# Optimization experiments

Measured on AMD Instinct MI355X. Metric: run time of the kernel, lower is better.

## Reference

```python
import jax, jax.numpy as jnp
import numpy as np

N_NODES = 100000
N_EDGES = 600000
H = 128          # hidden_units
LH = 256         # lin_hidden_units
F_IN = 3         # num_features (x, y, area)
C = 8            # out_classes


def setup_inputs() -> dict:
    key = jax.random.key(0)
    ks = jax.random.split(key, 12)
    s = 0.05
    return {
        "x": jax.random.normal(ks[0], (N_NODES, F_IN), dtype=jnp.float32),
        "edge_index": jax.random.randint(ks[1], (2, N_EDGES), 0, N_NODES, dtype=jnp.int64),
        # conv1: lin_l (aggregated neighbors, has bias), lin_r (root, no bias)
        "Wl1": jax.random.normal(ks[2], (H, F_IN), dtype=jnp.float32) * s,
        "bl1": jnp.zeros((H,), dtype=jnp.float32),
        "Wr1": jax.random.normal(ks[3], (H, F_IN), dtype=jnp.float32) * s,
        # conv2
        "Wl2": jax.random.normal(ks[4], (H, H), dtype=jnp.float32) * s,
        "bl2": jnp.zeros((H,), dtype=jnp.float32),
        "Wr2": jax.random.normal(ks[5], (H, H), dtype=jnp.float32) * s,
        # MLP head
        "W1": jax.random.normal(ks[6], (LH, H), dtype=jnp.float32) * s,
        "b1": jnp.zeros((LH,), dtype=jnp.float32),
        "W2": jax.random.normal(ks[7], (C, LH), dtype=jnp.float32) * s,
        "b2": jnp.zeros((C,), dtype=jnp.float32),
    }


def _normalize(x):
    coords = x[:, :2]                      # [N, 2]
    areas = x[:, 2:3]                      # [N, 1]
    mx = jnp.max(coords, axis=0)
    mn = jnp.min(coords, axis=0)
    theta = jnp.float32(np.pi / 2)
    c, sn = jnp.cos(theta), jnp.sin(theta)
    R = jnp.array([[1.0, 0.0], [0.0, 1.0]], dtype=x.dtype) * c + \
        jnp.array([[0.0, -1.0], [1.0, 0.0]], dtype=x.dtype) * sn
    rotated = coords @ R.T                 # (R @ coords.T).T
    rotate = (mx[1] - mn[1]) > (mx[0] - mn[0])
    coords = jnp.where(rotate, rotated, coords)
    coords = (coords - jnp.mean(coords, axis=0)) / jnp.max(coords, axis=0)
    areas = areas / jnp.max(areas, axis=0)
    return jnp.concatenate([coords, areas], axis=-1)


def _sage_conv(x, src, dst, Wl, bl, Wr):
    # mean aggregation of source features at target nodes
    msg = x[src]                                               # [E, d] gather
    agg = jax.ops.segment_sum(msg, dst, num_segments=N_NODES)  # [N, d]
    deg = jax.ops.segment_sum(jnp.ones((src.shape[0],), x.dtype), dst,
                              num_segments=N_NODES)
    agg = agg / jnp.maximum(deg, 1.0)[:, None]
    return agg @ Wl.T + bl + x @ Wr.T


def reference(x, edge_index, Wl1, bl1, Wr1, Wl2, bl2, Wr2, W1, b1, W2, b2):
    src, dst = edge_index[0], edge_index[1]
    h = _normalize(x)
    h = jnp.tanh(_sage_conv(h, src, dst, Wl1, bl1, Wr1))
    h = jnp.tanh(_sage_conv(h, src, dst, Wl2, bl2, Wr2))
    h = jnp.tanh(h @ W1.T + b1)
    h = h @ W2.T + b2
    return jax.nn.softmax(h, axis=1)
```

## Files before the change

### kernel.cpp

```cpp
#include <hip/hip_runtime.h>
#include <hip/hip_bf16.h>
#include <math.h>

#define N_NODES 100000
#define N_EDGES 600000
#define H 128
#define LH 256
#define CDIM 8
#define NB_STATS 256
#define NT128 ((N_NODES + 127) / 128)
#define ELLW 64
#define NB_NODE ((N_NODES + 255) / 256)

#define NBUCK 391
#define NBLK_P1 64
#define EPB (N_EDGES / NBLK_P1)
#define CAP 72

typedef __attribute__((ext_vector_type(8))) short short8;
typedef __attribute__((ext_vector_type(4))) float floatx4;

#define OFF_PART   0
#define OFF_DEG    2816
#define OFF_H0     (OFF_DEG + N_NODES)
#define OFF_ELL    (OFF_H0 + N_NODES*4)
#define OFF_CNTT   (OFF_ELL + N_NODES*ELLW)
#define OFF_SCR    (OFF_CNTT + NBUCK*NBLK_P1)
#define OFF_WPK2   (OFF_SCR + NBUCK*NBLK_P1*CAP*2)
#define OFF_WPK1   (OFF_WPK2 + 16384)
#define OFF_W2PK   (OFF_WPK1 + 16384)
#define OFF_XB     (OFF_W2PK + 2048)

__device__ __forceinline__ float rot_c() { return cosf(1.57079632679489661923f); }
__device__ __forceinline__ float rot_s() { return sinf(1.57079632679489661923f); }
__device__ __forceinline__ float bfhi(unsigned v) { return __uint_as_float(v & 0xffff0000u); }
__device__ __forceinline__ float bflo(unsigned v) { return __uint_as_float(v << 16); }
__device__ __forceinline__ unsigned short bfu(float f) {
    __hip_bfloat16 h = __float2bfloat16(f);
    return *(unsigned short*)&h;
}
__device__ __forceinline__ float ftanh(float x) {
    float e = __expf(2.0f * x);
    return 1.0f - 2.0f * __builtin_amdgcn_rcpf(e + 1.0f);
}

__global__ __launch_bounds__(256) void statsPart_k(const float* __restrict__ x,
        float* __restrict__ part, const int* __restrict__ ei,
        int* __restrict__ cntT, int2* __restrict__ scratch) {
    __shared__ float red[4][11];
    __shared__ int lcnt[NBUCK];
    int tid = threadIdx.x;

    if (blockIdx.x >= NB_STATS) {
        int blk = blockIdx.x - NB_STATS;
        for (int i = tid; i < NBUCK; i += 256) lcnt[i] = 0;
        __syncthreads();
        int base = blk * EPB;
        for (int e = base + tid; e < base + EPB; e += 256) {
            int s = ei[e], d = ei[N_EDGES + e];
            int b = d >> 8;
            int pos = atomicAdd(&lcnt[b], 1);
            scratch[(b * NBLK_P1 + blk) * CAP + pos] = make_int2(s, d);
        }
        __syncthreads();
        for (int i = tid; i < NBUCK; i += 256)
            cntT[i * NBLK_P1 + blk] = lcnt[i];
        return;
    }

    const float c = rot_c(), sn = rot_s();
    float mn0 = INFINITY, mx0 = -INFINITY, mn1 = INFINITY, mx1 = -INFINITY;
    float s0 = 0.f, s1 = 0.f, sr0 = 0.f, sr1 = 0.f;
    float mxr0 = -INFINITY, mxr1 = -INFINITY, mxa = -INFINITY;
    for (int i = blockIdx.x * 256 + tid; i < N_NODES; i += NB_STATS * 256) {
        float x0 = x[3*i], x1 = x[3*i+1], a = x[3*i+2];
        float r0 = c*x0 - sn*x1;
        float r1 = sn*x0 + c*x1;
        mn0 = fminf(mn0, x0); mx0 = fmaxf(mx0, x0);
        mn1 = fminf(mn1, x1); mx1 = fmaxf(mx1, x1);
        s0 += x0; s1 += x1; sr0 += r0; sr1 += r1;
        mxr0 = fmaxf(mxr0, r0); mxr1 = fmaxf(mxr1, r1);
        mxa = fmaxf(mxa, a);
    }
    float vals[11] = {mn0, mx0, mn1, mx1, s0, s1, sr0, sr1, mxr0, mxr1, mxa};
    int lane = tid & 63, wave = tid >> 6;
    #pragma unroll
    for (int v = 0; v < 11; v++) {
        const int op = (v==0||v==2) ? 0 : (v>=4 && v<=7) ? 2 : 1;
        float val = vals[v];
        #pragma unroll
        for (int off = 32; off > 0; off >>= 1) {
            float o = __shfl_down(val, off);
            val = (op==0) ? fminf(val,o) : (op==1) ? fmaxf(val,o) : (val+o);
        }
        if (lane == 0) red[wave][v] = val;
    }
    __syncthreads();
    if (tid < 11) {
        int v = tid;
        int op = (v==0||v==2) ? 0 : (v>=4 && v<=7) ? 2 : 1;
        float a = red[0][v], b = red[1][v], cc = red[2][v], d = red[3][v];
        float r = (op==0) ? fminf(fminf(a,b), fminf(cc,d))
                : (op==1) ? fmaxf(fmaxf(a,b), fmaxf(cc,d))
                : (a + b + cc + d);
        part[blockIdx.x * 11 + v] = r;
    }
}

__global__ __launch_bounds__(256) void binNorm_k(const float* __restrict__ x,
        const float* __restrict__ part, float4* __restrict__ h0,
        const float* __restrict__ Wl2, const float* __restrict__ Wr2,
        const float* __restrict__ W1, const float* __restrict__ W2,
        __hip_bfloat16* __restrict__ Wpk2, __hip_bfloat16* __restrict__ Wpk1,
        __hip_bfloat16* __restrict__ W2pk,
        const int* __restrict__ cntT, const int2* __restrict__ scratch,
        int* __restrict__ ell, int* __restrict__ deg) {
    __shared__ int pref[NBLK_P1 + 1];
    __shared__ int ncnt[256];
    __shared__ float res[11];
    int tid = threadIdx.x;

    if (blockIdx.x < NBUCK) {
        int b = blockIdx.x;
        ncnt[tid] = 0;
        if (tid < NBLK_P1) pref[tid + 1] = cntT[b * NBLK_P1 + tid];
        __syncthreads();
        if (tid == 0) {
            pref[0] = 0;
            int acc = 0;
            #pragma unroll 8
            for (int j = 0; j < NBLK_P1; j++) { acc += pref[j+1]; pref[j+1] = acc; }
        }
        __syncthreads();
        int T = pref[NBLK_P1];
        for (int f = tid; f < T; f += 256) {
            int lo = 0, hi = NBLK_P1;
            while (hi - lo > 1) {
                int mid = (lo + hi) >> 1;
                if (pref[mid] <= f) lo = mid; else hi = mid;
            }
            int2 sd = scratch[(b * NBLK_P1 + lo) * CAP + (f - pref[lo])];
            int pos = atomicAdd(&ncnt[sd.y & 255], 1);
            ell[(sd.y << 6) + pos] = sd.x;
        }
        __syncthreads();
        int n = (b << 8) + tid;
        if (n < N_NODES) deg[n] = ncnt[tid];
        return;
    }

    int nb = blockIdx.x - NBUCK;
    int i = nb * 256 + tid;
    if (tid < 64) {
        const int ops[11] = {0,1,0,1,2,2,2,2,1,1,1};
        for (int v = 0; v < 11; v++) {
            float val = part[tid * 11 + v];
            #pragma unroll
            for (int p = 1; p < 4; p++) {
                float o = part[(tid + p*64) * 11 + v];
                val = (ops[v]==0) ? fminf(val,o) : (ops[v]==1) ? fmaxf(val,o) : (val+o);
            }
            #pragma unroll
            for (int off = 32; off > 0; off >>= 1) {
                float o = __shfl_down(val, off);
                val = (ops[v]==0) ? fminf(val,o) : (ops[v]==1) ? fmaxf(val,o) : (val+o);
            }
            if (tid == 0) res[v] = val;
        }
    }
    __syncthreads();
    int rotate = (res[3] - res[2]) > (res[1] - res[0]);
    float mean0 = (rotate ? res[6] : res[4]) / (float)N_NODES;
    float mean1 = (rotate ? res[7] : res[5]) / (float)N_NODES;
    float imx0  = 1.0f / (rotate ? res[8] : res[1]);
    float imx1  = 1.0f / (rotate ? res[9] : res[3]);
    float imxa  = 1.0f / res[10];

    if (i < N_NODES) {
        const float c = rot_c(), sn = rot_s();
        float x0 = x[3*i], x1 = x[3*i+1], a = x[3*i+2];
        float u0 = rotate ? (c*x0 - sn*x1) : x0;
        float u1 = rotate ? (sn*x0 + c*x1) : x1;
        h0[i] = make_float4((u0 - mean0) * imx0, (u1 - mean1) * imx1, a * imxa, 0.f);
    }
    int idx = i;
    if (idx < 32768) {
        int j = idx & 7, lane = (idx >> 3) & 63, nt = (idx >> 9) & 7, ks = idx >> 12;
        int k = ks*32 + (lane >> 4)*8 + j;
        int n = nt*16 + (lane & 15);
        float v = (k < 128) ? Wl2[n*H + k] : Wr2[n*H + (k - 128)];
        Wpk2[idx] = __float2bfloat16(v);
    } else if (idx < 65536) {
        int i2 = idx - 32768;
        int j = i2 & 7, lane = (i2 >> 3) & 63, nt = (i2 >> 9) & 15, ks = i2 >> 13;
        int k = ks*32 + (lane >> 4)*8 + j;
        int n = nt*16 + (lane & 15);
        Wpk1[i2] = __float2bfloat16(W1[n*H + k]);
    } else if (idx < 69632) {
        int i3 = idx - 65536;
        int j = i3 & 7, lane = (i3 >> 3) & 63, ks = i3 >> 9;
        int k = ks*32 + (lane >> 4)*8 + j;
        int n = lane & 15;
        W2pk[i3] = __float2bfloat16((n < CDIM) ? W2[n*LH + k] : 0.f);
    }
}

__global__ __launch_bounds__(256) void agg1conv1_k(const float4* __restrict__ h0,
        const int* __restrict__ deg, const int* __restrict__ ell,
        const float* __restrict__ Wl1, const float* __restrict__ bl1,
        const float* __restrict__ Wr1, __hip_bfloat16* __restrict__ Xb) {
    __shared__ float wl[H*3], wr[H*3], bb[H];
    __shared__ float4 sa[256];
    int tid = threadIdx.x;
    for (int i = tid; i < H*3; i += 256) { wl[i] = Wl1[i]; wr[i] = Wr1[i]; }
    if (tid < H) bb[tid] = bl1[tid];
    int base = blockIdx.x * 256;
    int n = base + tid;
    float4 av = make_float4(0.f, 0.f, 0.f, 0.f);
    if (n < N_NODES) {
        int dg = deg[n];
        int start = n << 6, end = start + dg;
        float a0 = 0.f, a1 = 0.f, a2 = 0.f;
        int e = start;
        for (; e + 3 < end; e += 4) {
            int s0 = ell[e], s1 = ell[e+1], s2 = ell[e+2], s3 = ell[e+3];
            float4 v0 = h0[s0];
            float4 v1 = h0[s1];
            float4 v2 = h0[s2];
            float4 v3 = h0[s3];
            a0 += (v0.x + v1.x) + (v2.x + v3.x);
            a1 += (v0.y + v1.y) + (v2.y + v3.y);
            a2 += (v0.z + v1.z) + (v2.z + v3.z);
        }
        for (; e < end; e++) {
            float4 v = h0[ell[e]];
            a0 += v.x; a1 += v.y; a2 += v.z;
        }
        float inv = 1.0f / (float)max(dg, 1);
        av = make_float4(a0 * inv, a1 * inv, a2 * inv, 0.f);
    }
    sa[tid] = av;
    __syncthreads();
    int sub = tid >> 6;
    int j2 = (tid & 63) * 2;
    for (int i = 0; i < 64; i++) {
        int loc = i * 4 + sub;
        int nn = base + loc;
        if (nn >= N_NODES) break;
        float4 a = sa[loc];
        float4 xv = h0[nn];
        float o0 = wl[3*j2+0]*a.x + wl[3*j2+1]*a.y + wl[3*j2+2]*a.z + bb[j2]
                 + wr[3*j2+0]*xv.x + wr[3*j2+1]*xv.y + wr[3*j2+2]*xv.z;
        float o1 = wl[3*j2+3]*a.x + wl[3*j2+4]*a.y + wl[3*j2+5]*a.z + bb[j2+1]
                 + wr[3*j2+3]*xv.x + wr[3*j2+4]*xv.y + wr[3*j2+5]*xv.z;
        unsigned pv = ((unsigned)bfu(ftanh(o1)) << 16) | (unsigned)bfu(ftanh(o0));
        *(unsigned*)&Xb[(size_t)nn*256 + 128 + j2] = pv;
    }
}

__global__ void agg2_k(__hip_bfloat16* __restrict__ Xb, const int* __restrict__ deg,
                       const int* __restrict__ ell) {
    int lane = threadIdx.x & 15;
    int n = blockIdx.x * 16 + (threadIdx.x >> 4);
    int dg = deg[n];
    int start = n << 6, end = start + dg;
    const short* XbS = (const short*)Xb;
    float a0=0.f,a1=0.f,a2=0.f,a3=0.f,a4=0.f,a5=0.f,a6=0.f,a7=0.f;
    int e = start;
    for (; e + 1 < end; e += 2) {
        int s0 = ell[e], s1 = ell[e+1];
        uint4 v0 = *(const uint4*)&XbS[(size_t)s0*256 + 128 + lane*8];
        uint4 v1 = *(const uint4*)&XbS[(size_t)s1*256 + 128 + lane*8];
        a0 += bflo(v0.x) + bflo(v1.x); a1 += bfhi(v0.x) + bfhi(v1.x);
        a2 += bflo(v0.y) + bflo(v1.y); a3 += bfhi(v0.y) + bfhi(v1.y);
        a4 += bflo(v0.z) + bflo(v1.z); a5 += bfhi(v0.z) + bfhi(v1.z);
        a6 += bflo(v0.w) + bflo(v1.w); a7 += bfhi(v0.w) + bfhi(v1.w);
    }
    if (e < end) {
        int s0 = ell[e];
        uint4 v0 = *(const uint4*)&XbS[(size_t)s0*256 + 128 + lane*8];
        a0 += bflo(v0.x); a1 += bfhi(v0.x);
        a2 += bflo(v0.y); a3 += bfhi(v0.y);
        a4 += bflo(v0.z); a5 += bfhi(v0.z);
        a6 += bflo(v0.w); a7 += bfhi(v0.w);
    }
    float inv = 1.0f / (float)max(dg, 1);
    uint4 o;
    o.x = ((unsigned)bfu(a1*inv) << 16) | (unsigned)bfu(a0*inv);
    o.y = ((unsigned)bfu(a3*inv) << 16) | (unsigned)bfu(a2*inv);
    o.z = ((unsigned)bfu(a5*inv) << 16) | (unsigned)bfu(a4*inv);
    o.w = ((unsigned)bfu(a7*inv) << 16) | (unsigned)bfu(a6*inv);
    *(uint4*)&Xb[(size_t)n*256 + lane*8] = o;
}

__global__ __launch_bounds__(512, 4) void conv2mlp_k(const __hip_bfloat16* __restrict__ Xb,
        const __hip_bfloat16* __restrict__ Wpk2, const float* __restrict__ bl2,
        const __hip_bfloat16* __restrict__ Wpk1, const float* __restrict__ b1,
        const __hip_bfloat16* __restrict__ W2pk, const float* __restrict__ b2,
        float* __restrict__ out) {
    __shared__ short Cs[8 * 16 * 128];
    int tid = threadIdx.x;
    int lane = tid & 63, wave = tid >> 6;
    int quad = lane >> 4, m = lane & 15, c0 = lane & 15;
    short* Tw = &Cs[wave * (16 * 128)];
    const short* Bg2 = (const short*)Wpk2;
    const short* Bg1 = (const short*)Wpk1;
    const short* Bg0 = (const short*)W2pk;

    int tile = blockIdx.x;
    short8 areg[8];
    {
        int row = tile*128 + wave*16 + m;
        int rowL = row < N_NODES ? row : N_NODES - 1;
        const short* Arow = (const short*)Xb + (size_t)rowL * 256;
        #pragma unroll
        for (int ks = 0; ks < 8; ks++)
            areg[ks] = *(const short8*)(Arow + ks*32 + quad*8);
    }
    floatx4 acc2[8];
    #pragma unroll
    for (int i = 0; i < 8; i++)
        #pragma unroll
        for (int r = 0; r < 4; r++) acc2[i][r] = 0.f;
    #pragma unroll
    for (int ks = 0; ks < 8; ks++) {
        #pragma unroll
        for (int nt = 0; nt < 8; nt++) {
            short8 b = *(const short8*)&Bg2[((ks*8 + nt)*64 + lane)*8];
            acc2[nt] = __builtin_amdgcn_mfma_f32_16x16x32_bf16(areg[ks], b, acc2[nt], 0, 0, 0);
        }
    }
    #pragma unroll
    for (int nt = 0; nt < 8; nt++) {
        float bl2v = bl2[nt*16 + c0];
        int cg = nt*2 + (c0 >> 3);
        #pragma unroll
        for (int r = 0; r < 4; r++) {
            int row = quad*4 + r;
            Tw[row*128 + ((cg ^ row) << 3) + (c0 & 7)] =
                (short)bfu(ftanh(acc2[nt][r] + bl2v));
        }
    }
    floatx4 acc1[16];
    #pragma unroll
    for (int i = 0; i < 16; i++)
        #pragma unroll
        for (int r = 0; r < 4; r++) acc1[i][r] = 0.f;
    #pragma unroll
    for (int ks = 0; ks < 4; ks++) {
        short8 a = *(const short8*)&Tw[m*128 + (((ks*4 + quad) ^ m) << 3)];
        #pragma unroll
        for (int nt = 0; nt < 16; nt++) {
            short8 b = *(const short8*)&Bg1[((ks*16 + nt)*64 + lane)*8];
            acc1[nt] = __builtin_amdgcn_mfma_f32_16x16x32_bf16(a, b, acc1[nt], 0, 0, 0);
        }
    }
    floatx4 lacc;
    #pragma unroll
    for (int r = 0; r < 4; r++) lacc[r] = 0.f;
    #pragma unroll
    for (int ch = 0; ch < 4; ch++) {
        #pragma unroll
        for (int ntl = 0; ntl < 4; ntl++) {
            int nt = ch*4 + ntl;
            float b1v = b1[nt*16 + c0];
            int cg = ntl*2 + (c0 >> 3);
            #pragma unroll
            for (int r = 0; r < 4; r++) {
                int row = quad*4 + r;
                Tw[row*128 + ((cg ^ row) << 3) + (c0 & 7)] =
                    (short)bfu(ftanh(acc1[nt][r] + b1v));
            }
        }
        #pragma unroll
        for (int k2 = 0; k2 < 2; k2++) {
            short8 a = *(const short8*)&Tw[m*128 + (((k2*4 + quad) ^ m) << 3)];
            short8 w2 = *(const short8*)&Bg0[((ch*2 + k2)*64 + lane)*8];
            lacc = __builtin_amdgcn_mfma_f32_16x16x32_bf16(a, w2, lacc, 0, 0, 0);
        }
    }
    float b2v = (c0 < CDIM) ? b2[c0] : 0.f;
    int rbase = tile*128 + wave*16 + quad*4;
    #pragma unroll
    for (int r = 0; r < 4; r++) {
        float v = lacc[r] + b2v;
        float mval = (c0 < CDIM) ? v : -INFINITY;
        #pragma unroll
        for (int off = 1; off < 8; off <<= 1)
            mval = fmaxf(mval, __shfl_xor(mval, off));
        float e = (c0 < CDIM) ? __expf(v - mval) : 0.f;
        float ssum = e;
        #pragma unroll
        for (int off = 1; off < 8; off <<= 1)
            ssum += __shfl_xor(ssum, off);
        int rowg = rbase + r;
        if (c0 < CDIM && rowg < N_NODES)
            out[(size_t)rowg*CDIM + c0] = e / ssum;
    }
}

extern "C" void kernel_launch(void* const* d_in, const int* in_sizes, int n_in,
                              void* d_out, int out_size, void* d_ws, size_t ws_size,
                              hipStream_t stream) {
    const float* x   = (const float*)d_in[0];
    const int*   ei  = (const int*)d_in[1];
    const float* Wl1 = (const float*)d_in[2];
    const float* bl1 = (const float*)d_in[3];
    const float* Wr1 = (const float*)d_in[4];
    const float* Wl2 = (const float*)d_in[5];
    const float* bl2 = (const float*)d_in[6];
    const float* Wr2 = (const float*)d_in[7];
    const float* W1  = (const float*)d_in[8];
    const float* b1  = (const float*)d_in[9];
    const float* W2  = (const float*)d_in[10];
    const float* b2  = (const float*)d_in[11];

    float* ws     = (float*)d_ws;
    float* part   = ws + OFF_PART;
    int*   deg    = (int*)(ws + OFF_DEG);
    float4* h0    = (float4*)(ws + OFF_H0);
    int*   ell    = (int*)(ws + OFF_ELL);
    int*   cntT   = (int*)(ws + OFF_CNTT);
    int2*  scratch= (int2*)(ws + OFF_SCR);
    __hip_bfloat16* Wpk2 = (__hip_bfloat16*)(ws + OFF_WPK2);
    __hip_bfloat16* Wpk1 = (__hip_bfloat16*)(ws + OFF_WPK1);
    __hip_bfloat16* W2pk = (__hip_bfloat16*)(ws + OFF_W2PK);
    __hip_bfloat16* Xb   = (__hip_bfloat16*)(ws + OFF_XB);

    statsPart_k<<<NB_STATS + NBLK_P1, 256, 0, stream>>>(x, part, ei, cntT, scratch);
    binNorm_k<<<NBUCK + NB_NODE, 256, 0, stream>>>(x, part, h0,
            Wl2, Wr2, W1, W2, Wpk2, Wpk1, W2pk, cntT, scratch, ell, deg);
    agg1conv1_k<<<NB_NODE, 256, 0, stream>>>(h0, deg, ell,
            Wl1, bl1, Wr1, Xb);
    agg2_k<<<N_NODES / 16, 256, 0, stream>>>(Xb, deg, ell);
    conv2mlp_k<<<NT128, 512, 0, stream>>>(Xb, Wpk2, bl2, Wpk1, b1, W2pk, b2,
            (float*)d_out);
}
```

Before: 219.5 us.

## Stage W1 weights in LDS and shrink per-wave activation staging to padded slices

Each block now copies the packed 64KB W1 weight matrix into shared memory once, so MLP layer-1 B operands come from LDS rather than global memory. The conv2 and layer-1 tanh outputs are written to LDS in 32-column chunks, each just before the MFMA k-step that reads it, using a 40-short padded row stride instead of a full 128-wide swizzled tile. This cuts per-wave staging memory and interleaves the activation math with the matmuls. The cost is about 74KB of shared memory per block, which likely lowers occupancy below the launch-bounds target, plus an extra block-wide sync for the weight copy.

```diff
diff --git a/kernel.cpp b/kernel.cpp
--- a/kernel.cpp
+++ b/kernel.cpp
@@ -293,18 +293,26 @@
     *(uint4*)&Xb[(size_t)n*256 + lane*8] = o;
 }
 
+#define SLICE 640
 __global__ __launch_bounds__(512, 4) void conv2mlp_k(const __hip_bfloat16* __restrict__ Xb,
         const __hip_bfloat16* __restrict__ Wpk2, const float* __restrict__ bl2,
         const __hip_bfloat16* __restrict__ Wpk1, const float* __restrict__ b1,
         const __hip_bfloat16* __restrict__ W2pk, const float* __restrict__ b2,
         float* __restrict__ out) {
-    __shared__ short Cs[8 * 16 * 128];
+    __shared__ short Ws1[32768];
+    __shared__ short Cs[8 * SLICE];
     int tid = threadIdx.x;
     int lane = tid & 63, wave = tid >> 6;
     int quad = lane >> 4, m = lane & 15, c0 = lane & 15;
-    short* Tw = &Cs[wave * (16 * 128)];
+    {
+        const float4* s1 = (const float4*)Wpk1;
+        float4* d1 = (float4*)Ws1;
+        #pragma unroll
+        for (int i = 0; i < 8; i++) d1[tid + i*512] = s1[tid + i*512];
+    }
+    __syncthreads();
+    short* Tw = &Cs[wave * SLICE];
     const short* Bg2 = (const short*)Wpk2;
-    const short* Bg1 = (const short*)Wpk1;
     const short* Bg0 = (const short*)W2pk;
 
     int tile = blockIdx.x;
@@ -330,17 +338,6 @@
             acc2[nt] = __builtin_amdgcn_mfma_f32_16x16x32_bf16(areg[ks], b, acc2[nt], 0, 0, 0);
         }
     }
-    #pragma unroll
-    for (int nt = 0; nt < 8; nt++) {
-        float bl2v = bl2[nt*16 + c0];
-        int cg = nt*2 + (c0 >> 3);
-        #pragma unroll
-        for (int r = 0; r < 4; r++) {
-            int row = quad*4 + r;
-            Tw[row*128 + ((cg ^ row) << 3) + (c0 & 7)] =
-                (short)bfu(ftanh(acc2[nt][r] + bl2v));
-        }
-    }
     floatx4 acc1[16];
     #pragma unroll
     for (int i = 0; i < 16; i++)
@@ -348,10 +345,19 @@
         for (int r = 0; r < 4; r++) acc1[i][r] = 0.f;
     #pragma unroll
     for (int ks = 0; ks < 4; ks++) {
-        short8 a = *(const short8*)&Tw[m*128 + (((ks*4 + quad) ^ m) << 3)];
+        #pragma unroll
+        for (int p = 0; p < 2; p++) {
+            int nt = ks*2 + p;
+            float bl2v = bl2[nt*16 + c0];
+            int lc = p*16 + c0;
+            #pragma unroll
+            for (int r = 0; r < 4; r++)
+                Tw[(quad*4 + r)*40 + lc] = (short)bfu(ftanh(acc2[nt][r] + bl2v));
+        }
+        short8 a = *(const short8*)&Tw[m*40 + quad*8];
         #pragma unroll
         for (int nt = 0; nt < 16; nt++) {
-            short8 b = *(const short8*)&Bg1[((ks*16 + nt)*64 + lane)*8];
+            short8 b = *(const short8*)&Ws1[((ks*16 + nt)*64 + lane)*8];
             acc1[nt] = __builtin_amdgcn_mfma_f32_16x16x32_bf16(a, b, acc1[nt], 0, 0, 0);
         }
     }
@@ -359,25 +365,19 @@
     #pragma unroll
     for (int r = 0; r < 4; r++) lacc[r] = 0.f;
     #pragma unroll
-    for (int ch = 0; ch < 4; ch++) {
-        #pragma unroll
-        for (int ntl = 0; ntl < 4; ntl++) {
-            int nt = ch*4 + ntl;
+    for (int ch = 0; ch < 8; ch++) {
+        #pragma unroll
+        for (int p = 0; p < 2; p++) {
+            int nt = ch*2 + p;
             float b1v = b1[nt*16 + c0];
-            int cg = ntl*2 + (c0 >> 3);
+            int lc = p*16 + c0;
             #pragma unroll
-            for (int r = 0; r < 4; r++) {
-                int row = quad*4 + r;
-                Tw[row*128 + ((cg ^ row) << 3) + (c0 & 7)] =
-                    (short)bfu(ftanh(acc1[nt][r] + b1v));
-            }
-        }
-        #pragma unroll
-        for (int k2 = 0; k2 < 2; k2++) {
-            short8 a = *(const short8*)&Tw[m*128 + (((k2*4 + quad) ^ m) << 3)];
-            short8 w2 = *(const short8*)&Bg0[((ch*2 + k2)*64 + lane)*8];
-            lacc = __builtin_amdgcn_mfma_f32_16x16x32_bf16(a, w2, lacc, 0, 0, 0);
-        }
+            for (int r = 0; r < 4; r++)
+                Tw[(quad*4 + r)*40 + lc] = (short)bfu(ftanh(acc1[nt][r] + b1v));
+        }
+        short8 a = *(const short8*)&Tw[m*40 + quad*8];
+        short8 w2 = *(const short8*)&Bg0[(ch*64 + lane)*8];
+        lacc = __builtin_amdgcn_mfma_f32_16x16x32_bf16(a, w2, lacc, 0, 0, 0);
     }
     float b2v = (c0 < CDIM) ? b2[c0] : 0.f;
     int rbase = tile*128 + wave*16 + quad*4;
```

After: 209.4 us. 1.05x faster.

## Process two 16-row groups per wave in conv2+MLP kernel to reuse weight fragments

Applied to the files above, without the earlier changes.

The fused conv2+MLP kernel now launches 256 threads per block, and each wave handles 32 rows as two 16-row groups. Every weight B-fragment loaded from global memory feeds two MFMAs, which halves weight load traffic per row. The 256-wide hidden layer is split into two passes of 128 columns, and each 32-column slice is staged through a small per-wave LDS buffer so the W2 projection runs incrementally. The cost is more accumulator registers per wave and lower occupancy (launch bounds 256,2), which can limit latency hiding.

```diff
diff --git a/kernel.cpp b/kernel.cpp
--- a/kernel.cpp
+++ b/kernel.cpp
@@ -293,41 +293,45 @@
     *(uint4*)&Xb[(size_t)n*256 + lane*8] = o;
 }
 
-__global__ __launch_bounds__(512, 4) void conv2mlp_k(const __hip_bfloat16* __restrict__ Xb,
+__global__ __launch_bounds__(256, 2) void conv2mlp_k(const __hip_bfloat16* __restrict__ Xb,
         const __hip_bfloat16* __restrict__ Wpk2, const float* __restrict__ bl2,
         const __hip_bfloat16* __restrict__ Wpk1, const float* __restrict__ b1,
         const __hip_bfloat16* __restrict__ W2pk, const float* __restrict__ b2,
         float* __restrict__ out) {
-    __shared__ short Cs[8 * 16 * 128];
+    __shared__ short Hs[4 * 2 * 2048];
+    __shared__ short Ms[4 * 640];
     int tid = threadIdx.x;
     int lane = tid & 63, wave = tid >> 6;
     int quad = lane >> 4, m = lane & 15, c0 = lane & 15;
-    short* Tw = &Cs[wave * (16 * 128)];
+    short* Hw = &Hs[wave * 4096];
+    short* Tw = &Ms[wave * 640];
     const short* Bg2 = (const short*)Wpk2;
     const short* Bg1 = (const short*)Wpk1;
     const short* Bg0 = (const short*)W2pk;
 
     int tile = blockIdx.x;
-    short8 areg[8];
-    {
-        int row = tile*128 + wave*16 + m;
-        int rowL = row < N_NODES ? row : N_NODES - 1;
-        const short* Arow = (const short*)Xb + (size_t)rowL * 256;
-        #pragma unroll
-        for (int ks = 0; ks < 8; ks++)
-            areg[ks] = *(const short8*)(Arow + ks*32 + quad*8);
-    }
-    floatx4 acc2[8];
+    int rbase0 = tile*128 + wave*32;
+    int r0 = rbase0 + m;            r0 = r0 < N_NODES ? r0 : N_NODES - 1;
+    int r1 = rbase0 + 16 + m;       r1 = r1 < N_NODES ? r1 : N_NODES - 1;
+    const short* Arow0 = (const short*)Xb + (size_t)r0 * 256;
+    const short* Arow1 = (const short*)Xb + (size_t)r1 * 256;
+
+    floatx4 acc2[8][2];
     #pragma unroll
     for (int i = 0; i < 8; i++)
         #pragma unroll
-        for (int r = 0; r < 4; r++) acc2[i][r] = 0.f;
+        for (int rg = 0; rg < 2; rg++)
+            #pragma unroll
+            for (int r = 0; r < 4; r++) acc2[i][rg][r] = 0.f;
     #pragma unroll
     for (int ks = 0; ks < 8; ks++) {
+        short8 a0 = *(const short8*)(Arow0 + ks*32 + quad*8);
+        short8 a1 = *(const short8*)(Arow1 + ks*32 + quad*8);
         #pragma unroll
         for (int nt = 0; nt < 8; nt++) {
             short8 b = *(const short8*)&Bg2[((ks*8 + nt)*64 + lane)*8];
-            acc2[nt] = __builtin_amdgcn_mfma_f32_16x16x32_bf16(areg[ks], b, acc2[nt], 0, 0, 0);
+            acc2[nt][0] = __builtin_amdgcn_mfma_f32_16x16x32_bf16(a0, b, acc2[nt][0], 0, 0, 0);
+            acc2[nt][1] = __builtin_amdgcn_mfma_f32_16x16x32_bf16(a1, b, acc2[nt][1], 0, 0, 0);
         }
     }
     #pragma unroll
@@ -335,67 +339,82 @@
         float bl2v = bl2[nt*16 + c0];
         int cg = nt*2 + (c0 >> 3);
         #pragma unroll
-        for (int r = 0; r < 4; r++) {
-            int row = quad*4 + r;
-            Tw[row*128 + ((cg ^ row) << 3) + (c0 & 7)] =
-                (short)bfu(ftanh(acc2[nt][r] + bl2v));
-        }
-    }
-    floatx4 acc1[16];
-    #pragma unroll
-    for (int i = 0; i < 16; i++)
-        #pragma unroll
-        for (int r = 0; r < 4; r++) acc1[i][r] = 0.f;
-    #pragma unroll
-    for (int ks = 0; ks < 4; ks++) {
-        short8 a = *(const short8*)&Tw[m*128 + (((ks*4 + quad) ^ m) << 3)];
-        #pragma unroll
-        for (int nt = 0; nt < 16; nt++) {
-            short8 b = *(const short8*)&Bg1[((ks*16 + nt)*64 + lane)*8];
-            acc1[nt] = __builtin_amdgcn_mfma_f32_16x16x32_bf16(a, b, acc1[nt], 0, 0, 0);
-        }
-    }
-    floatx4 lacc;
-    #pragma unroll
-    for (int r = 0; r < 4; r++) lacc[r] = 0.f;
-    #pragma unroll
-    for (int ch = 0; ch < 4; ch++) {
-        #pragma unroll
-        for (int ntl = 0; ntl < 4; ntl++) {
-            int nt = ch*4 + ntl;
-            float b1v = b1[nt*16 + c0];
-            int cg = ntl*2 + (c0 >> 3);
+        for (int rg = 0; rg < 2; rg++) {
+            short* Hrg = Hw + rg*2048;
             #pragma unroll
             for (int r = 0; r < 4; r++) {
                 int row = quad*4 + r;
-                Tw[row*128 + ((cg ^ row) << 3) + (c0 & 7)] =
-                    (short)bfu(ftanh(acc1[nt][r] + b1v));
-            }
-        }
-        #pragma unroll
-        for (int k2 = 0; k2 < 2; k2++) {
-            short8 a = *(const short8*)&Tw[m*128 + (((k2*4 + quad) ^ m) << 3)];
-            short8 w2 = *(const short8*)&Bg0[((ch*2 + k2)*64 + lane)*8];
-            lacc = __builtin_amdgcn_mfma_f32_16x16x32_bf16(a, w2, lacc, 0, 0, 0);
+                Hrg[row*128 + ((cg ^ row) << 3) + (c0 & 7)] =
+                    (short)bfu(ftanh(acc2[nt][rg][r] + bl2v));
+            }
+        }
+    }
+    floatx4 lacc[2];
+    #pragma unroll
+    for (int rg = 0; rg < 2; rg++)
+        #pragma unroll
+        for (int r = 0; r < 4; r++) lacc[rg][r] = 0.f;
+    #pragma unroll
+    for (int p = 0; p < 2; p++) {
+        floatx4 acc1[8][2];
+        #pragma unroll
+        for (int i = 0; i < 8; i++)
+            #pragma unroll
+            for (int rg = 0; rg < 2; rg++)
+                #pragma unroll
+                for (int r = 0; r < 4; r++) acc1[i][rg][r] = 0.f;
+        #pragma unroll
+        for (int ks = 0; ks < 4; ks++) {
+            short8 a0 = *(const short8*)&Hw[0*2048 + m*128 + (((ks*4 + quad) ^ m) << 3)];
+            short8 a1 = *(const short8*)&Hw[1*2048 + m*128 + (((ks*4 + quad) ^ m) << 3)];
+            #pragma unroll
+            for (int ntl = 0; ntl < 8; ntl++) {
+                int nt = p*8 + ntl;
+                short8 b = *(const short8*)&Bg1[((ks*16 + nt)*64 + lane)*8];
+                acc1[ntl][0] = __builtin_amdgcn_mfma_f32_16x16x32_bf16(a0, b, acc1[ntl][0], 0, 0, 0);
+                acc1[ntl][1] = __builtin_amdgcn_mfma_f32_16x16x32_bf16(a1, b, acc1[ntl][1], 0, 0, 0);
+            }
+        }
+        #pragma unroll
+        for (int ch = 0; ch < 4; ch++) {
+            short8 w2 = *(const short8*)&Bg0[((p*4 + ch)*64 + lane)*8];
+            #pragma unroll
+            for (int rg = 0; rg < 2; rg++) {
+                #pragma unroll
+                for (int l = 0; l < 2; l++) {
+                    int ntl = ch*2 + l;
+                    float b1v = b1[(p*8 + ntl)*16 + c0];
+                    int lc = l*16 + c0;
+                    #pragma unroll
+                    for (int r = 0; r < 4; r++)
+                        Tw[(quad*4 + r)*40 + lc] =
+                            (short)bfu(ftanh(acc1[ntl][rg][r] + b1v));
+                }
+                short8 a = *(const short8*)&Tw[m*40 + quad*8];
+                lacc[rg] = __builtin_amdgcn_mfma_f32_16x16x32_bf16(a, w2, lacc[rg], 0, 0, 0);
+            }
         }
     }
     float b2v = (c0 < CDIM) ? b2[c0] : 0.f;
-    int rbase = tile*128 + wave*16 + quad*4;
-    #pragma unroll
-    for (int r = 0; r < 4; r++) {
-        float v = lacc[r] + b2v;
-        float mval = (c0 < CDIM) ? v : -INFINITY;
-        #pragma unroll
-        for (int off = 1; off < 8; off <<= 1)
-            mval = fmaxf(mval, __shfl_xor(mval, off));
-        float e = (c0 < CDIM) ? __expf(v - mval) : 0.f;
-        float ssum = e;
-        #pragma unroll
-        for (int off = 1; off < 8; off <<= 1)
-            ssum += __shfl_xor(ssum, off);
-        int rowg = rbase + r;
-        if (c0 < CDIM && rowg < N_NODES)
-            out[(size_t)rowg*CDIM + c0] = e / ssum;
+    #pragma unroll
+    for (int rg = 0; rg < 2; rg++) {
+        int rbase = rbase0 + rg*16 + quad*4;
+        #pragma unroll
+        for (int r = 0; r < 4; r++) {
+            float v = lacc[rg][r] + b2v;
+            float mval = (c0 < CDIM) ? v : -INFINITY;
+            #pragma unroll
+            for (int off = 1; off < 8; off <<= 1)
+                mval = fmaxf(mval, __shfl_xor(mval, off));
+            float e = (c0 < CDIM) ? __expf(v - mval) : 0.f;
+            float ssum = e;
+            #pragma unroll
+            for (int off = 1; off < 8; off <<= 1)
+                ssum += __shfl_xor(ssum, off);
+            int rowg = rbase + r;
+            if (c0 < CDIM && rowg < N_NODES)
+                out[(size_t)rowg*CDIM + c0] = e / ssum;
+        }
     }
 }
 
@@ -433,6 +452,6 @@
     agg1conv1_k<<<NB_NODE, 256, 0, stream>>>(h0, deg, ell,
             Wl1, bl1, Wr1, Xb);
     agg2_k<<<N_NODES / 16, 256, 0, stream>>>(Xb, deg, ell);
-    conv2mlp_k<<<NT128, 512, 0, stream>>>(Xb, Wpk2, bl2, Wpk1, b1, W2pk, b2,
+    conv2mlp_k<<<NT128, 256, 0, stream>>>(Xb, Wpk2, bl2, Wpk1, b1, W2pk, b2,
             (float*)d_out);
 }
```

Result: slower. 238.9 us (+8.8%).
